# Optimization experiments

Measured on AMD Instinct MI355X. Metric: run time of the kernel, lower is better.

## Reference

```python
import math
import jax
import jax.numpy as jnp
import numpy as np

B = 4096        # number of contexts / segments
T = 262144      # total objects across all segments (avg 64 per segment)
F = 128         # object_size
H = 256         # hidden_size
C = 512         # context_size


def setup_inputs() -> dict:
    key = jax.random.key(0)
    ks = jax.random.split(key, 8)
    objects = jax.random.normal(ks[0], (T, F), dtype=jnp.float32)
    context = jax.random.normal(ks[1], (B, C), dtype=jnp.float32)
    # sorted segment ids; guarantee every segment non-empty by seeding one id per segment
    extra = jax.random.randint(ks[2], (T - B,), 0, B)
    segment_ids = jnp.sort(jnp.concatenate([jnp.arange(B, dtype=extra.dtype), extra])).astype(jnp.int32)
    s = 0.05
    return {
        "objects": objects,
        "context": context,
        "segment_ids": segment_ids,
        "W1": jax.random.normal(ks[3], (F, H), dtype=jnp.float32) * s,
        "b1": jnp.zeros((H,), dtype=jnp.float32),
        "W2": jax.random.normal(ks[4], (H, H), dtype=jnp.float32) * s,
        "b2": jnp.zeros((H,), dtype=jnp.float32),
        "W3": jax.random.normal(ks[5], (H, 2 * H), dtype=jnp.float32) * s,
        "b3": jnp.zeros((2 * H,), dtype=jnp.float32),
        "Wq": jax.random.normal(ks[6], (C, H), dtype=jnp.float32) * s,
        "bq": jnp.zeros((H,), dtype=jnp.float32),
    }


def reference(objects, context, segment_ids, W1, b1, W2, b2, W3, b3, Wq, bq):
    num_segments = context.shape[0]
    # kv MLP: Linear -> ReLU -> Linear -> ReLU -> Linear(2H)
    h = jax.nn.relu(objects @ W1 + b1)
    h = jax.nn.relu(h @ W2 + b2)
    kv = h @ W3 + b3                                   # [T, 2H]
    k, v = jnp.split(kv, 2, axis=1)                    # [T, H] each
    # query per object via repeat_interleave == gather by segment id
    q = (context @ Wq + bq)[segment_ids]               # [T, H]
    logits = jnp.sum(q * k, axis=1) / math.sqrt(k.shape[1])   # [T]
    # per-segment stable softmax
    m = jax.ops.segment_max(logits, segment_ids, num_segments=num_segments)
    e = jnp.exp(logits - m[segment_ids])
    z = jax.ops.segment_sum(e, segment_ids, num_segments=num_segments)
    w = e / z[segment_ids]                             # [T]
    # per-segment weighted sum of values
    embedding = jax.ops.segment_sum(w[:, None] * v, segment_ids, num_segments=num_segments)  # [B, H]
    return embedding, w
```

## Files before the change

### kernel.cpp

```cpp
#include <hip/hip_runtime.h>
#include <hip/hip_bf16.h>

#define T_TOTAL 262144
#define B_SEG   4096

typedef __attribute__((ext_vector_type(8))) short short8;
typedef __attribute__((ext_vector_type(4))) float f32x4;

__device__ __forceinline__ short f2bf(float x) {
    __hip_bfloat16 h = __float2bfloat16(x);
    return *reinterpret_cast<short*>(&h);
}
__device__ __forceinline__ float bf2f(short s) {
    unsigned u = ((unsigned)(unsigned short)s) << 16;
    return __uint_as_float(u);
}

__global__ __launch_bounds__(256) void prep_all(
    const float* __restrict__ W1, const float* __restrict__ W2,
    const float* __restrict__ W3, const float* __restrict__ Wq,
    const float* __restrict__ bq, const float* __restrict__ b3,
    const float* __restrict__ ctx,
    short* __restrict__ W1T, short* __restrict__ W2T, short* __restrict__ W3vT,
    float* __restrict__ bz, float* __restrict__ wc, float* __restrict__ c0,
    float* __restrict__ Wqz, float* __restrict__ cbuf) {
    __shared__ __align__(16) char smem[33280];
    const int b = blockIdx.x, tid = threadIdx.x;

    if (b < 40) {
        float (*t)[68] = reinterpret_cast<float(*)[68]>(smem);
        const float* src; short* dst;
        int k0, n0_src, n0_dst, sstride, dstride;
        if (b < 8) {
            int kt = b >> 2, nt = b & 3;
            src = W1; dst = W1T; sstride = 256; dstride = 128;
            k0 = kt * 64; n0_src = nt * 64; n0_dst = nt * 64;
        } else if (b < 24) {
            int id = b - 8, kt = id >> 2, nt = id & 3;
            src = W2; dst = W2T; sstride = 256; dstride = 256;
            k0 = kt * 64; n0_src = nt * 64; n0_dst = nt * 64;
        } else {
            int id = b - 24, kt = id >> 2, nt = id & 3;
            src = W3; dst = W3vT; sstride = 512; dstride = 256;
            k0 = kt * 64; n0_src = 256 + nt * 64; n0_dst = nt * 64;
        }
        {
            int r = tid >> 4, c4 = (tid & 15) * 4;
#pragma unroll
            for (int p = 0; p < 4; p++) {
                int k = p * 16 + r;
                float4 v = *reinterpret_cast<const float4*>(
                    &src[(size_t)(k0 + k) * sstride + n0_src + c4]);
                *reinterpret_cast<float4*>(&t[k][c4]) = v;
            }
        }
        __syncthreads();
        {
            int n = tid >> 2, kq = tid & 3;
            short8 s0, s1;
#pragma unroll
            for (int i = 0; i < 8; i++) s0[i] = f2bf(t[kq * 16 + i][n]);
#pragma unroll
            for (int i = 0; i < 8; i++) s1[i] = f2bf(t[kq * 16 + 8 + i][n]);
            short* o = &dst[(size_t)(n0_dst + n) * dstride + k0 + kq * 16];
            *reinterpret_cast<short8*>(o) = s0;
            *reinterpret_cast<short8*>(o + 8) = s1;
        }
    } else if (b < 42) {
        if (b == 40) {
            float s = 0.f;
            for (int n = 0; n < 256; n += 4) {
                float4 a = *reinterpret_cast<const float4*>(&W3[(size_t)tid * 512 + n]);
                float4 v = *reinterpret_cast<const float4*>(&bq[n]);
                s += a.x * v.x + a.y * v.y + a.z * v.z + a.w * v.w;
            }
            bz[tid] = s;
        } else {
#pragma unroll
            for (int h = 0; h < 2; h++) {
                int c = h * 256 + tid;
                float s = 0.f;
                for (int n = 0; n < 256; n += 4) {
                    float4 a = *reinterpret_cast<const float4*>(&Wq[(size_t)c * 256 + n]);
                    float4 v = *reinterpret_cast<const float4*>(&b3[n]);
                    s += a.x * v.x + a.y * v.y + a.z * v.z + a.w * v.w;
                }
                wc[c] = s;
            }
            if (tid == 0) {
                float s = 0.f;
                for (int n = 0; n < 256; n++) s += bq[n] * b3[n];
                c0[0] = s;
            }
        }
    } else if (b < 554) {
        float (*wq)[260] = reinterpret_cast<float(*)[260]>(smem);
        float (*w3)[260] = reinterpret_cast<float(*)[260]>(smem + 16640);
        const int id = b - 42;
        const int c0r = (id >> 4) * 16, j0 = (id & 15) * 16;
        {
            int r = tid >> 4, nq = tid & 15;
#pragma unroll
            for (int p = 0; p < 4; p++) {
                int col = nq * 4 + p * 64;
                *reinterpret_cast<float4*>(&wq[r][col]) =
                    *reinterpret_cast<const float4*>(&Wq[(size_t)(c0r + r) * 256 + col]);
                *reinterpret_cast<float4*>(&w3[r][col]) =
                    *reinterpret_cast<const float4*>(&W3[(size_t)(j0 + r) * 512 + col]);
            }
        }
        __syncthreads();
        const int ci = tid >> 4, ji = tid & 15;
        float s = 0.f;
        for (int n = 0; n < 256; n += 4) {
            float4 a = *reinterpret_cast<const float4*>(&wq[ci][n]);
            float4 v = *reinterpret_cast<const float4*>(&w3[ji][n]);
            s += a.x * v.x + a.y * v.y + a.z * v.z + a.w * v.w;
        }
        Wqz[(size_t)(c0r + ci) * 256 + j0 + ji] = s;
    } else {
        const int id = b - 554;
        const int row = id * 32 + (tid >> 3);
        const int l = tid & 7;
        float s = 0.f;
        for (int i = 0; i < 64; i += 4) {
            float4 a = *reinterpret_cast<const float4*>(&ctx[(size_t)row * 512 + l * 64 + i]);
            float4 v = *reinterpret_cast<const float4*>(&wc[l * 64 + i]);
            s += a.x * v.x + a.y * v.y + a.z * v.z + a.w * v.w;
        }
        s += __shfl_xor(s, 1); s += __shfl_xor(s, 2); s += __shfl_xor(s, 4);
        if (l == 0) cbuf[row] = s + c0[0];
    }
}

__global__ __launch_bounds__(256) void zq_kernel(
    const float* __restrict__ ctx, const float* __restrict__ Wqz,
    const float* __restrict__ bz, float* __restrict__ zq) {
    __shared__ float As[2][16][68];
    const int tid = threadIdx.x;
    const int tm = tid & 15, tn = tid >> 4;
    const int row0 = blockIdx.x * 64, col0 = blockIdx.y * 64;
    const int lr = tid >> 2, lk = tid & 3;

    float acc[4][4];
#pragma unroll
    for (int i = 0; i < 4; i++)
#pragma unroll
        for (int j = 0; j < 4; j++) acc[i][j] = 0.f;

    float4 av = *reinterpret_cast<const float4*>(&ctx[(size_t)(row0 + lr) * 512 + lk * 4]);
    for (int c = 0; c < 32; c++) {
        int cur = c & 1;
        As[cur][lk * 4 + 0][lr] = av.x;
        As[cur][lk * 4 + 1][lr] = av.y;
        As[cur][lk * 4 + 2][lr] = av.z;
        As[cur][lk * 4 + 3][lr] = av.w;
        __syncthreads();
        if (c < 31)
            av = *reinterpret_cast<const float4*>(
                &ctx[(size_t)(row0 + lr) * 512 + (c + 1) * 16 + lk * 4]);
#pragma unroll
        for (int k = 0; k < 16; k++) {
            float4 a = *reinterpret_cast<const float4*>(&As[cur][k][tm * 4]);
            float4 b = *reinterpret_cast<const float4*>(
                &Wqz[(size_t)(c * 16 + k) * 256 + col0 + tn * 4]);
#pragma unroll
            for (int i = 0; i < 4; i++) {
                float ai = (i == 0) ? a.x : (i == 1) ? a.y : (i == 2) ? a.z : a.w;
                acc[i][0] += ai * b.x; acc[i][1] += ai * b.y;
                acc[i][2] += ai * b.z; acc[i][3] += ai * b.w;
            }
        }
    }
    float4 bv = *reinterpret_cast<const float4*>(&bz[col0 + tn * 4]);
#pragma unroll
    for (int i = 0; i < 4; i++) {
        float4 o = {acc[i][0] + bv.x, acc[i][1] + bv.y, acc[i][2] + bv.z, acc[i][3] + bv.w};
        *reinterpret_cast<float4*>(&zq[(size_t)(row0 + tm * 4 + i) * 256 + col0 + tn * 4]) = o;
    }
}

template <int K>
__device__ __forceinline__ void run_layer(
    const short* __restrict__ act, const short* __restrict__ Wt,
    int nbase, int l16, int quad, f32x4 acc[4][4]) {
    constexpr int KK = K / 32;
    const f32x4 zero = {0.f, 0.f, 0.f, 0.f};
#pragma unroll
    for (int i = 0; i < 4; i++)
#pragma unroll
        for (int j = 0; j < 4; j++) acc[i][j] = zero;

    int woff[4];
#pragma unroll
    for (int ns = 0; ns < 4; ns++)
        woff[ns] = ((nbase + ns * 16 + l16) * K + quad * 8) * 2;
    const int abase = l16 * K * 2;
    const char* actc = reinterpret_cast<const char*>(act);
    const char* wtc  = reinterpret_cast<const char*>(Wt);

    short8 wbuf[2][4];
    short8 areg[2][4];

    auto loadA = [&](int kk, int slot) {
        const int sg = (((kk * 4 + quad) ^ l16) * 16);
#pragma unroll
        for (int ms = 0; ms < 4; ms++)
            areg[slot][ms] = *reinterpret_cast<const short8*>(
                actc + abase + ms * 16 * K * 2 + sg);
    };
    auto loadW = [&](int kk, int slot) {
#pragma unroll
        for (int ns = 0; ns < 4; ns++)
            wbuf[slot][ns] = *reinterpret_cast<const short8*>(
                wtc + woff[ns] + kk * 64);
    };

    loadW(0, 0); loadA(0, 0);
    loadW(1, 1); loadA(1, 1);
#pragma unroll
    for (int kk = 0; kk < KK; kk++) {
        const int cur = kk & 1;
#pragma unroll
        for (int ms = 0; ms < 4; ms++)
#pragma unroll
            for (int ns = 0; ns < 4; ns++)
                acc[ms][ns] = __builtin_amdgcn_mfma_f32_16x16x32_bf16(
                    wbuf[cur][ns], areg[cur][ms], acc[ms][ns], 0, 0, 0);
        if (kk + 2 < KK) { loadW(kk + 2, cur); loadA(kk + 2, cur); }
    }
}

__global__ __launch_bounds__(256, 3) void mlp_kernel(
    const float* __restrict__ objects, const int* __restrict__ seg_ids,
    const short* __restrict__ W1T, const short* __restrict__ W2T,
    const short* __restrict__ W3vT,
    const float* __restrict__ b1, const float* __restrict__ b2,
    const float* __restrict__ b3,
    const float* __restrict__ zqbuf, const float* __restrict__ cbuf,
    float* __restrict__ logits_out, short* __restrict__ vout) {
    __shared__ __align__(16) short bufH[64 * 256];
    __shared__ float slots[4][64];

    const int tid  = threadIdx.x;
    const int wave = tid >> 6;
    const int lane = tid & 63;
    const int quad = lane >> 4;
    const int l16  = lane & 15;
    const int nbase = wave * 64;
    const int row0  = blockIdx.x * 64;

    {
        const float4* op = reinterpret_cast<const float4*>(objects + (size_t)row0 * 128);
#pragma unroll
        for (int i = 0; i < 4; i++) {
            int u = tid + i * 256;
            int m = u >> 4, kg = u & 15;
            float4 x0 = op[u * 2];
            float4 x1 = op[u * 2 + 1];
            short8 s;
            s[0] = f2bf(x0.x); s[1] = f2bf(x0.y); s[2] = f2bf(x0.z); s[3] = f2bf(x0.w);
            s[4] = f2bf(x1.x); s[5] = f2bf(x1.y); s[6] = f2bf(x1.z); s[7] = f2bf(x1.w);
            *reinterpret_cast<short8*>(&bufH[m * 128 + ((kg ^ (m & 15)) * 8)]) = s;
        }
    }
    __syncthreads();

    f32x4 acc[4][4];

    auto store_act = [&](const float* __restrict__ bias) {
#pragma unroll
        for (int ns = 0; ns < 4; ns++) {
            int n0 = nbase + ns * 16 + quad * 4;
            float4 bv = *reinterpret_cast<const float4*>(&bias[n0]);
#pragma unroll
            for (int ms = 0; ms < 4; ms++) {
                int m = ms * 16 + l16;
                short4 s;
                s.x = f2bf(fmaxf(acc[ms][ns][0] + bv.x, 0.f));
                s.y = f2bf(fmaxf(acc[ms][ns][1] + bv.y, 0.f));
                s.z = f2bf(fmaxf(acc[ms][ns][2] + bv.z, 0.f));
                s.w = f2bf(fmaxf(acc[ms][ns][3] + bv.w, 0.f));
                *reinterpret_cast<short4*>(
                    &bufH[m * 256 + (((n0 >> 3) ^ (m & 15)) * 8) + (n0 & 7)]) = s;
            }
        }
    };

    run_layer<128>(bufH, W1T, nbase, l16, quad, acc);
    __syncthreads();
    store_act(b1);
    __syncthreads();

    run_layer<256>(bufH, W2T, nbase, l16, quad, acc);
    __syncthreads();
    {
        float part[4] = {0.f, 0.f, 0.f, 0.f};
        int segm[4];
#pragma unroll
        for (int ms = 0; ms < 4; ms++) segm[ms] = seg_ids[row0 + ms * 16 + l16];
#pragma unroll
        for (int ns = 0; ns < 4; ns++) {
            int n0 = nbase + ns * 16 + quad * 4;
            float4 bv = *reinterpret_cast<const float4*>(&b2[n0]);
#pragma unroll
            for (int ms = 0; ms < 4; ms++) {
                int m = ms * 16 + l16;
                float h0 = fmaxf(acc[ms][ns][0] + bv.x, 0.f);
                float h1v = fmaxf(acc[ms][ns][1] + bv.y, 0.f);
                float h2v = fmaxf(acc[ms][ns][2] + bv.z, 0.f);
                float h3 = fmaxf(acc[ms][ns][3] + bv.w, 0.f);
                short4 s;
                s.x = f2bf(h0); s.y = f2bf(h1v); s.z = f2bf(h2v); s.w = f2bf(h3);
                *reinterpret_cast<short4*>(
                    &bufH[m * 256 + (((n0 >> 3) ^ (m & 15)) * 8) + (n0 & 7)]) = s;
                float4 zq4 = *reinterpret_cast<const float4*>(
                    &zqbuf[(size_t)segm[ms] * 256 + n0]);
                part[ms] += h0 * zq4.x + h1v * zq4.y + h2v * zq4.z + h3 * zq4.w;
            }
        }
#pragma unroll
        for (int ms = 0; ms < 4; ms++) {
            float p = part[ms];
            p += __shfl_xor(p, 16);
            p += __shfl_xor(p, 32);
            if (quad == 0) slots[wave][ms * 16 + l16] = p;
        }
    }
    __syncthreads();
    if (tid < 64) {
        int seg = seg_ids[row0 + tid];
        float s = slots[0][tid] + slots[1][tid] + slots[2][tid] + slots[3][tid] + cbuf[seg];
        logits_out[row0 + tid] = s * 0.0625f;
    }

    run_layer<256>(bufH, W3vT, nbase, l16, quad, acc);
    __syncthreads();
#pragma unroll
    for (int ns = 0; ns < 4; ns++) {
        int n0 = nbase + ns * 16 + quad * 4;
        float4 bv = *reinterpret_cast<const float4*>(&b3[256 + n0]);
#pragma unroll
        for (int ms = 0; ms < 4; ms++) {
            int m = ms * 16 + l16;
            short4 s;
            s.x = f2bf(acc[ms][ns][0] + bv.x);
            s.y = f2bf(acc[ms][ns][1] + bv.y);
            s.z = f2bf(acc[ms][ns][2] + bv.z);
            s.w = f2bf(acc[ms][ns][3] + bv.w);
            *reinterpret_cast<short4*>(
                &bufH[m * 256 + (((n0 >> 3) ^ (m & 15)) * 8) + (n0 & 7)]) = s;
        }
    }
    __syncthreads();
#pragma unroll
    for (int i = 0; i < 8; i++) {
        int idx = tid + i * 256;
        int m = idx >> 5, sg = idx & 31;
        short8 val = *reinterpret_cast<const short8*>(&bufH[m * 256 + sg * 8]);
        int n0 = (sg ^ (m & 15)) * 8;
        *reinterpret_cast<short8*>(&vout[(size_t)(row0 + m) * 256 + n0]) = val;
    }
}

__global__ __launch_bounds__(256) void seg_starts_kernel(
    const int* __restrict__ seg, int* __restrict__ starts) {
    int t = blockIdx.x * 256 + threadIdx.x;
    if (t >= T_TOTAL) return;
    int s = seg[t];
    if (t == 0) {
        for (int q = 0; q <= s; q++) starts[q] = 0;
    } else {
        int p = seg[t - 1];
        for (int q = p + 1; q <= s; q++) starts[q] = t;
    }
}

__global__ __launch_bounds__(64) void segment_kernel(
    const float* __restrict__ logits, const short* __restrict__ vbuf,
    const int* __restrict__ starts, float* __restrict__ emb,
    float* __restrict__ wout) {
    const int b = blockIdx.x;
    const int lane = threadIdx.x;
    const int start = starts[b];
    const int end = (b == B_SEG - 1) ? T_TOTAL : starts[b + 1];

    float mx = -1e30f;
    for (int t = start + lane; t < end; t += 64) mx = fmaxf(mx, logits[t]);
#pragma unroll
    for (int off = 32; off >= 1; off >>= 1) mx = fmaxf(mx, __shfl_xor(mx, off));

    float s = 0.f;
    for (int t = start + lane; t < end; t += 64) s += __expf(logits[t] - mx);
#pragma unroll
    for (int off = 32; off >= 1; off >>= 1) s += __shfl_xor(s, off);
    const float invz = 1.f / s;

    for (int t = start + lane; t < end; t += 64)
        wout[t] = __expf(logits[t] - mx) * invz;

    float a[4][4];
#pragma unroll
    for (int i = 0; i < 4; i++)
#pragma unroll
        for (int j = 0; j < 4; j++) a[i][j] = 0.f;

    int t = start;
    for (; t + 8 <= end; t += 8) {
#pragma unroll
        for (int u = 0; u < 8; u++) {
            float wv = __expf(logits[t + u] - mx) * invz;
            short4 v4 = *reinterpret_cast<const short4*>(
                &vbuf[(size_t)(t + u) * 256 + lane * 4]);
            a[u & 3][0] += wv * bf2f(v4.x);
            a[u & 3][1] += wv * bf2f(v4.y);
            a[u & 3][2] += wv * bf2f(v4.z);
            a[u & 3][3] += wv * bf2f(v4.w);
        }
    }
    for (; t < end; t++) {
        float wv = __expf(logits[t] - mx) * invz;
        short4 v4 = *reinterpret_cast<const short4*>(
            &vbuf[(size_t)t * 256 + lane * 4]);
        a[0][0] += wv * bf2f(v4.x);
        a[0][1] += wv * bf2f(v4.y);
        a[0][2] += wv * bf2f(v4.z);
        a[0][3] += wv * bf2f(v4.w);
    }
    float4 o;
    o.x = a[0][0] + a[1][0] + a[2][0] + a[3][0];
    o.y = a[0][1] + a[1][1] + a[2][1] + a[3][1];
    o.z = a[0][2] + a[1][2] + a[2][2] + a[3][2];
    o.w = a[0][3] + a[1][3] + a[2][3] + a[3][3];
    *reinterpret_cast<float4*>(&emb[(size_t)b * 256 + lane * 4]) = o;
}

extern "C" void kernel_launch(void* const* d_in, const int* in_sizes, int n_in,
                              void* d_out, int out_size, void* d_ws, size_t ws_size,
                              hipStream_t stream) {
    const float* objects = (const float*)d_in[0];
    const float* context = (const float*)d_in[1];
    const int*   seg     = (const int*)d_in[2];
    const float* W1 = (const float*)d_in[3];
    const float* b1 = (const float*)d_in[4];
    const float* W2 = (const float*)d_in[5];
    const float* b2 = (const float*)d_in[6];
    const float* W3 = (const float*)d_in[7];
    const float* b3 = (const float*)d_in[8];
    const float* Wq = (const float*)d_in[9];
    const float* bq = (const float*)d_in[10];

    char* ws = (char*)d_ws;
    float* zqbuf = (float*)(ws);
    float* cbuf  = (float*)(ws + 4194304);
    int*   seg_starts = (int*)(ws + 4194304);
    short* W1T   = (short*)(ws + 4210688);
    short* W2T   = (short*)(ws + 4276224);
    short* W3vT  = (short*)(ws + 4407296);
    char*  lreg   = ws + 4538368;
    float* logits = (float*)lreg;
    float* Wqz    = (float*)lreg;
    float* bz     = (float*)(lreg + 524288);
    float* wc     = (float*)(lreg + 525312);
    float* c0     = (float*)(lreg + 527360);
    short* vbuf   = (short*)(ws + 5586944);

    float* emb  = (float*)d_out;
    float* wout = emb + (size_t)B_SEG * 256;

    prep_all<<<682, 256, 0, stream>>>(W1, W2, W3, Wq, bq, b3, context,
                                      W1T, W2T, W3vT, bz, wc, c0, Wqz, cbuf);
    zq_kernel<<<dim3(64, 4), 256, 0, stream>>>(context, Wqz, bz, zqbuf);
    mlp_kernel<<<T_TOTAL / 64, 256, 0, stream>>>(objects, seg, W1T, W2T, W3vT,
                                                 b1, b2, b3, zqbuf, cbuf,
                                                 logits, vbuf);
    seg_starts_kernel<<<T_TOTAL / 256, 256, 0, stream>>>(seg, seg_starts);
    segment_kernel<<<B_SEG, 64, 0, stream>>>(logits, vbuf, seg_starts, emb, wout);
}
```

Measured before the change: 450.9 us.

## Fold segment-start computation into prep kernel and retune zq, V store, segment reduce

Moves the segment-start scan into extra blocks of the prep kernel, removing one launch. The zq GEMM now uses 32-row tiles with 4x2 outputs per thread, doubling the grid for more parallelism. The MLP kernel writes bf16 V directly to global memory instead of staging it through swizzled shared memory, which drops two barriers at the cost of less coalesced 8-byte stores. The segment kernel splits rows between two half-waves with 16-byte loads and combines them with a shuffle. Workspace offsets are moved so seg_starts no longer overlaps cbuf.

```diff
diff --git a/kernel.cpp b/kernel.cpp
--- a/kernel.cpp
+++ b/kernel.cpp
@@ -20,10 +20,11 @@
     const float* __restrict__ W1, const float* __restrict__ W2,
     const float* __restrict__ W3, const float* __restrict__ Wq,
     const float* __restrict__ bq, const float* __restrict__ b3,
-    const float* __restrict__ ctx,
+    const float* __restrict__ ctx, const int* __restrict__ seg,
     short* __restrict__ W1T, short* __restrict__ W2T, short* __restrict__ W3vT,
     float* __restrict__ bz, float* __restrict__ wc, float* __restrict__ c0,
-    float* __restrict__ Wqz, float* __restrict__ cbuf) {
+    float* __restrict__ Wqz, float* __restrict__ cbuf,
+    int* __restrict__ starts) {
     __shared__ __align__(16) char smem[33280];
     const int b = blockIdx.x, tid = threadIdx.x;
 
@@ -118,7 +119,7 @@
             s += a.x * v.x + a.y * v.y + a.z * v.z + a.w * v.w;
         }
         Wqz[(size_t)(c0r + ci) * 256 + j0 + ji] = s;
-    } else {
+    } else if (b < 682) {
         const int id = b - 554;
         const int row = id * 32 + (tid >> 3);
         const int l = tid & 7;
@@ -130,53 +131,59 @@
         }
         s += __shfl_xor(s, 1); s += __shfl_xor(s, 2); s += __shfl_xor(s, 4);
         if (l == 0) cbuf[row] = s + c0[0];
+    } else {
+        int t = (b - 682) * 256 + tid;
+        if (t < T_TOTAL) {
+            int s = seg[t];
+            if (t == 0) {
+                for (int q = 0; q <= s; q++) starts[q] = 0;
+            } else {
+                int p = seg[t - 1];
+                for (int q = p + 1; q <= s; q++) starts[q] = t;
+            }
+        }
     }
 }
 
 __global__ __launch_bounds__(256) void zq_kernel(
     const float* __restrict__ ctx, const float* __restrict__ Wqz,
     const float* __restrict__ bz, float* __restrict__ zq) {
-    __shared__ float As[2][16][68];
+    __shared__ float As[2][16][44];
     const int tid = threadIdx.x;
-    const int tm = tid & 15, tn = tid >> 4;
-    const int row0 = blockIdx.x * 64, col0 = blockIdx.y * 64;
-    const int lr = tid >> 2, lk = tid & 3;
-
-    float acc[4][4];
-#pragma unroll
-    for (int i = 0; i < 4; i++)
-#pragma unroll
-        for (int j = 0; j < 4; j++) acc[i][j] = 0.f;
-
-    float4 av = *reinterpret_cast<const float4*>(&ctx[(size_t)(row0 + lr) * 512 + lk * 4]);
+    const int tm = tid & 7, tn = tid >> 3;
+    const int row0 = blockIdx.x * 32, col0 = blockIdx.y * 64;
+    const int lr = tid >> 3, lk = tid & 7;
+
+    float acc[4][2];
+#pragma unroll
+    for (int i = 0; i < 4; i++) { acc[i][0] = 0.f; acc[i][1] = 0.f; }
+
+    float2 av = *reinterpret_cast<const float2*>(&ctx[(size_t)(row0 + lr) * 512 + lk * 2]);
     for (int c = 0; c < 32; c++) {
         int cur = c & 1;
-        As[cur][lk * 4 + 0][lr] = av.x;
-        As[cur][lk * 4 + 1][lr] = av.y;
-        As[cur][lk * 4 + 2][lr] = av.z;
-        As[cur][lk * 4 + 3][lr] = av.w;
+        As[cur][lk * 2 + 0][lr] = av.x;
+        As[cur][lk * 2 + 1][lr] = av.y;
         __syncthreads();
         if (c < 31)
-            av = *reinterpret_cast<const float4*>(
-                &ctx[(size_t)(row0 + lr) * 512 + (c + 1) * 16 + lk * 4]);
+            av = *reinterpret_cast<const float2*>(
+                &ctx[(size_t)(row0 + lr) * 512 + (c + 1) * 16 + lk * 2]);
 #pragma unroll
         for (int k = 0; k < 16; k++) {
             float4 a = *reinterpret_cast<const float4*>(&As[cur][k][tm * 4]);
-            float4 b = *reinterpret_cast<const float4*>(
-                &Wqz[(size_t)(c * 16 + k) * 256 + col0 + tn * 4]);
-#pragma unroll
-            for (int i = 0; i < 4; i++) {
-                float ai = (i == 0) ? a.x : (i == 1) ? a.y : (i == 2) ? a.z : a.w;
-                acc[i][0] += ai * b.x; acc[i][1] += ai * b.y;
-                acc[i][2] += ai * b.z; acc[i][3] += ai * b.w;
-            }
-        }
-    }
-    float4 bv = *reinterpret_cast<const float4*>(&bz[col0 + tn * 4]);
+            float2 b = *reinterpret_cast<const float2*>(
+                &Wqz[(size_t)(c * 16 + k) * 256 + col0 + tn * 2]);
+            acc[0][0] += a.x * b.x; acc[0][1] += a.x * b.y;
+            acc[1][0] += a.y * b.x; acc[1][1] += a.y * b.y;
+            acc[2][0] += a.z * b.x; acc[2][1] += a.z * b.y;
+            acc[3][0] += a.w * b.x; acc[3][1] += a.w * b.y;
+        }
+    }
+    float2 bv = *reinterpret_cast<const float2*>(&bz[col0 + tn * 2]);
 #pragma unroll
     for (int i = 0; i < 4; i++) {
-        float4 o = {acc[i][0] + bv.x, acc[i][1] + bv.y, acc[i][2] + bv.z, acc[i][3] + bv.w};
-        *reinterpret_cast<float4*>(&zq[(size_t)(row0 + tm * 4 + i) * 256 + col0 + tn * 4]) = o;
+        float2 o = {acc[i][0] + bv.x, acc[i][1] + bv.y};
+        *reinterpret_cast<float2*>(
+            &zq[(size_t)(row0 + tm * 4 + i) * 256 + col0 + tn * 2]) = o;
     }
 }
 
@@ -335,7 +342,6 @@
     }
 
     run_layer<256>(bufH, W3vT, nbase, l16, quad, acc);
-    __syncthreads();
 #pragma unroll
     for (int ns = 0; ns < 4; ns++) {
         int n0 = nbase + ns * 16 + quad * 4;
@@ -349,30 +355,8 @@
             s.z = f2bf(acc[ms][ns][2] + bv.z);
             s.w = f2bf(acc[ms][ns][3] + bv.w);
             *reinterpret_cast<short4*>(
-                &bufH[m * 256 + (((n0 >> 3) ^ (m & 15)) * 8) + (n0 & 7)]) = s;
-        }
-    }
-    __syncthreads();
-#pragma unroll
-    for (int i = 0; i < 8; i++) {
-        int idx = tid + i * 256;
-        int m = idx >> 5, sg = idx & 31;
-        short8 val = *reinterpret_cast<const short8*>(&bufH[m * 256 + sg * 8]);
-        int n0 = (sg ^ (m & 15)) * 8;
-        *reinterpret_cast<short8*>(&vout[(size_t)(row0 + m) * 256 + n0]) = val;
-    }
-}
-
-__global__ __launch_bounds__(256) void seg_starts_kernel(
-    const int* __restrict__ seg, int* __restrict__ starts) {
-    int t = blockIdx.x * 256 + threadIdx.x;
-    if (t >= T_TOTAL) return;
-    int s = seg[t];
-    if (t == 0) {
-        for (int q = 0; q <= s; q++) starts[q] = 0;
-    } else {
-        int p = seg[t - 1];
-        for (int q = p + 1; q <= s; q++) starts[q] = t;
+                &vout[(size_t)(row0 + m) * 256 + n0]) = s;
+        }
     }
 }
 
@@ -399,40 +383,48 @@
     for (int t = start + lane; t < end; t += 64)
         wout[t] = __expf(logits[t] - mx) * invz;
 
-    float a[4][4];
-#pragma unroll
-    for (int i = 0; i < 4; i++)
-#pragma unroll
-        for (int j = 0; j < 4; j++) a[i][j] = 0.f;
+    const int half = lane >> 5;
+    const int c8 = (lane & 31) * 8;
+    float a[4][8];
+#pragma unroll
+    for (int u = 0; u < 4; u++)
+#pragma unroll
+        for (int j = 0; j < 8; j++) a[u][j] = 0.f;
 
     int t = start;
     for (; t + 8 <= end; t += 8) {
 #pragma unroll
-        for (int u = 0; u < 8; u++) {
-            float wv = __expf(logits[t + u] - mx) * invz;
-            short4 v4 = *reinterpret_cast<const short4*>(
-                &vbuf[(size_t)(t + u) * 256 + lane * 4]);
-            a[u & 3][0] += wv * bf2f(v4.x);
-            a[u & 3][1] += wv * bf2f(v4.y);
-            a[u & 3][2] += wv * bf2f(v4.z);
-            a[u & 3][3] += wv * bf2f(v4.w);
-        }
-    }
-    for (; t < end; t++) {
-        float wv = __expf(logits[t] - mx) * invz;
-        short4 v4 = *reinterpret_cast<const short4*>(
-            &vbuf[(size_t)t * 256 + lane * 4]);
-        a[0][0] += wv * bf2f(v4.x);
-        a[0][1] += wv * bf2f(v4.y);
-        a[0][2] += wv * bf2f(v4.z);
-        a[0][3] += wv * bf2f(v4.w);
-    }
-    float4 o;
-    o.x = a[0][0] + a[1][0] + a[2][0] + a[3][0];
-    o.y = a[0][1] + a[1][1] + a[2][1] + a[3][1];
-    o.z = a[0][2] + a[1][2] + a[2][2] + a[3][2];
-    o.w = a[0][3] + a[1][3] + a[2][3] + a[3][3];
-    *reinterpret_cast<float4*>(&emb[(size_t)b * 256 + lane * 4]) = o;
+        for (int u = 0; u < 4; u++) {
+            int row = t + u * 2 + half;
+            float wv = __expf(logits[row] - mx) * invz;
+            short8 v8 = *reinterpret_cast<const short8*>(
+                &vbuf[(size_t)row * 256 + c8]);
+#pragma unroll
+            for (int j = 0; j < 8; j++) a[u][j] += wv * bf2f(v8[j]);
+        }
+    }
+    for (; t < end; t += 2) {
+        int row = t + half;
+        if (row < end) {
+            float wv = __expf(logits[row] - mx) * invz;
+            short8 v8 = *reinterpret_cast<const short8*>(
+                &vbuf[(size_t)row * 256 + c8]);
+#pragma unroll
+            for (int j = 0; j < 8; j++) a[0][j] += wv * bf2f(v8[j]);
+        }
+    }
+    float o[8];
+#pragma unroll
+    for (int j = 0; j < 8; j++) {
+        o[j] = a[0][j] + a[1][j] + a[2][j] + a[3][j];
+        o[j] += __shfl_xor(o[j], 32);
+    }
+    if (half == 0) {
+        float4 o0 = {o[0], o[1], o[2], o[3]};
+        float4 o1 = {o[4], o[5], o[6], o[7]};
+        *reinterpret_cast<float4*>(&emb[(size_t)b * 256 + c8]) = o0;
+        *reinterpret_cast<float4*>(&emb[(size_t)b * 256 + c8 + 4]) = o1;
+    }
 }
 
 extern "C" void kernel_launch(void* const* d_in, const int* in_sizes, int n_in,
@@ -453,27 +445,27 @@
     char* ws = (char*)d_ws;
     float* zqbuf = (float*)(ws);
     float* cbuf  = (float*)(ws + 4194304);
-    int*   seg_starts = (int*)(ws + 4194304);
-    short* W1T   = (short*)(ws + 4210688);
-    short* W2T   = (short*)(ws + 4276224);
-    short* W3vT  = (short*)(ws + 4407296);
-    char*  lreg   = ws + 4538368;
+    int*   seg_starts = (int*)(ws + 4227072);
+    short* W1T   = (short*)(ws + 4259840);
+    short* W2T   = (short*)(ws + 4325376);
+    short* W3vT  = (short*)(ws + 4456448);
+    char*  lreg   = ws + 4587520;
     float* logits = (float*)lreg;
     float* Wqz    = (float*)lreg;
     float* bz     = (float*)(lreg + 524288);
     float* wc     = (float*)(lreg + 525312);
     float* c0     = (float*)(lreg + 527360);
-    short* vbuf   = (short*)(ws + 5586944);
+    short* vbuf   = (short*)(ws + 5636096);
 
     float* emb  = (float*)d_out;
     float* wout = emb + (size_t)B_SEG * 256;
 
-    prep_all<<<682, 256, 0, stream>>>(W1, W2, W3, Wq, bq, b3, context,
-                                      W1T, W2T, W3vT, bz, wc, c0, Wqz, cbuf);
-    zq_kernel<<<dim3(64, 4), 256, 0, stream>>>(context, Wqz, bz, zqbuf);
+    prep_all<<<1706, 256, 0, stream>>>(W1, W2, W3, Wq, bq, b3, context, seg,
+                                       W1T, W2T, W3vT, bz, wc, c0, Wqz, cbuf,
+                                       seg_starts);
+    zq_kernel<<<dim3(128, 4), 256, 0, stream>>>(context, Wqz, bz, zqbuf);
     mlp_kernel<<<T_TOTAL / 64, 256, 0, stream>>>(objects, seg, W1T, W2T, W3vT,
                                                  b1, b2, b3, zqbuf, cbuf,
                                                  logits, vbuf);
-    seg_starts_kernel<<<T_TOTAL / 256, 256, 0, stream>>>(seg, seg_starts);
     segment_kernel<<<B_SEG, 64, 0, stream>>>(logits, vbuf, seg_starts, emb, wout);
 }
```

Result: slower. 467.1 us (+3.6%).
